# Optimization experiments

Hardware: AMD Instinct MI355X
Metric: run time of the kernel (lower is better)

Reference implementation:

```python
import jax, jax.numpy as jnp
import numpy as np

N_QUBITS = 7
N_LAYERS = 4
DIM = 2 ** N_QUBITS  # 128
# PennyLane StronglyEntanglingLayers default ranges: (l % (n_wires-1)) + 1
RANGES = [(l % (N_QUBITS - 1)) + 1 for l in range(N_LAYERS)]  # [1,2,3,4]
BATCH = 262144


def rot_matrix(phi, theta, omega):
    """PennyLane Rot(phi, theta, omega) = RZ(omega) RY(theta) RZ(phi)."""
    c = jnp.cos(theta / 2)
    s = jnp.sin(theta / 2)
    a = jnp.exp(-0.5j * (phi + omega)) * c
    b = -jnp.exp(0.5j * (phi - omega)) * s
    cc = jnp.exp(-0.5j * (phi - omega)) * s
    d = jnp.exp(0.5j * (phi + omega)) * c
    return jnp.stack([jnp.stack([a, b]), jnp.stack([cc, d])])  # (2,2) complex64


def apply_1q(psi, U, wire):
    # psi: (batch, 2,2,2,2,2,2,2); apply 2x2 U on qubit axis 1+wire
    psi = jnp.moveaxis(psi, 1 + wire, -1)
    psi = psi @ U.T
    return jnp.moveaxis(psi, -1, 1 + wire)


def apply_cnot(psi, ctrl, tgt):
    psi = jnp.moveaxis(psi, (1 + ctrl, 1 + tgt), (-2, -1))
    # flip target amplitude pair where control == 1
    psi = jnp.concatenate([psi[..., 0:1, :], psi[..., 1:2, ::-1]], axis=-2)
    return jnp.moveaxis(psi, (-2, -1), (1 + ctrl, 1 + tgt))


def setup_inputs() -> dict:
    key = jax.random.key(0)
    k1, k2 = jax.random.split(key)
    x = jax.random.normal(k1, (BATCH, DIM), dtype=jnp.float32)
    weights = jax.random.normal(k2, (N_LAYERS, N_QUBITS, 3), dtype=jnp.float32)
    return {"x": x, "weights": weights}


def reference(x, weights):
    # AmplitudeEmbedding with normalize=True
    norm = jnp.linalg.norm(x, axis=-1, keepdims=True)
    psi = (x / norm).astype(jnp.complex64)
    psi = psi.reshape((-1,) + (2,) * N_QUBITS)

    # StronglyEntanglingLayers
    for l in range(N_LAYERS):
        for w in range(N_QUBITS):
            U = rot_matrix(weights[l, w, 0], weights[l, w, 1], weights[l, w, 2])
            psi = apply_1q(psi, U, w)
        r = RANGES[l]
        for w in range(N_QUBITS):
            psi = apply_cnot(psi, w, (w + r) % N_QUBITS)

    # expval(Z0 @ Z6): sign = (-1)^(b0 + b6)
    probs = (jnp.abs(psi) ** 2).reshape(-1, 2, DIM // 4, 2)  # (batch, q0, mid, q6)
    z = jnp.array([1.0, -1.0], dtype=jnp.float32)
    return jnp.einsum('a,namb,b->n', z, probs, z)
```

## Files before the change

### kernel.cpp

```cpp
#include <hip/hip_runtime.h>


#define N_QUBITS 7
#define DIM 128
#define N_LAYERS 4
#define BATCH 262144
#define GRID 512
#define ROWS 32
#define ITERS (BATCH / (GRID * ROWS))

typedef short short8 __attribute__((ext_vector_type(8)));
typedef float f32x4 __attribute__((ext_vector_type(4)));
typedef unsigned int u32;
typedef __attribute__((address_space(1))) const u32 g_u32;
typedef __attribute__((address_space(3))) u32 l_u32;

__device__ __forceinline__ unsigned short f2bf(float f) {
  unsigned u = __builtin_bit_cast(unsigned, f);
  u += 0x7fffu + ((u >> 16) & 1u);
  return (unsigned short)(u >> 16);
}

__device__ __forceinline__ unsigned pk2(float x, float y) {
  unsigned ux = __builtin_bit_cast(unsigned, x) + 0x8000u;
  unsigned uy = __builtin_bit_cast(unsigned, y) + 0x8000u;
  return __builtin_amdgcn_perm(uy, ux, 0x07060302u);
}

__device__ __forceinline__ short8 pack_bf16(float4 lo, float4 hi) {
  uint4 d;
  d.x = pk2(lo.x, lo.y);
  d.y = pk2(lo.z, lo.w);
  d.z = pk2(hi.x, hi.y);
  d.w = pk2(hi.z, hi.w);
  return __builtin_bit_cast(short8, d);
}

__global__ void sim_columns(const float* __restrict__ W,
                            float* __restrict__ Ur, float* __restrict__ Ui) {
  __shared__ float sr[DIM], si[DIM];
  const int c = blockIdx.x;
  const int t = threadIdx.x;

  sr[t] = (t == c) ? 1.f : 0.f;        si[t] = 0.f;
  sr[t + 64] = (t + 64 == c) ? 1.f : 0.f;  si[t + 64] = 0.f;
  __syncthreads();

  for (int l = 0; l < N_LAYERS; ++l) {
    for (int w = 0; w < N_QUBITS; ++w) {
      const float phi = W[(l * 7 + w) * 3 + 0];
      const float th  = W[(l * 7 + w) * 3 + 1];
      const float om  = W[(l * 7 + w) * 3 + 2];
      const float ch = __cosf(0.5f * th), sh = __sinf(0.5f * th);
      const float ap = 0.5f * (phi + om), am = 0.5f * (phi - om);
      const float cap = __cosf(ap), sap = __sinf(ap);
      const float cam = __cosf(am), sam = __sinf(am);
      const float ar =  cap * ch, ai = -sap * ch;
      const float br = -cam * sh, bi = -sam * sh;
      const float cr =  cam * sh, ci = -sam * sh;
      const float dr =  cap * ch, di =  sap * ch;

      const int m = 1 << (6 - w);
      const int i0 = ((t & ~(m - 1)) << 1) | (t & (m - 1));
      const int i1 = i0 | m;
      const float x0r = sr[i0], x0i = si[i0];
      const float x1r = sr[i1], x1i = si[i1];
      __syncthreads();
      sr[i0] = ar * x0r - ai * x0i + br * x1r - bi * x1i;
      si[i0] = ar * x0i + ai * x0r + br * x1i + bi * x1r;
      sr[i1] = cr * x0r - ci * x0i + dr * x1r - di * x1i;
      si[i1] = cr * x0i + ci * x0r + dr * x1i + di * x1r;
      __syncthreads();
    }
    const int r = (l % (N_QUBITS - 1)) + 1;
    for (int w = 0; w < N_QUBITS; ++w) {
      const int ctrl = w, tgt = (w + r) % N_QUBITS;
      const int cmask = 1 << (6 - ctrl), tmask = 1 << (6 - tgt);
      const int i0 = ((t & ~(tmask - 1)) << 1) | (t & (tmask - 1));
      const int i1 = i0 | tmask;
      const float a0r = sr[i0], a0i = si[i0];
      const float a1r = sr[i1], a1i = si[i1];
      __syncthreads();
      if (i0 & cmask) {
        sr[i0] = a1r; si[i0] = a1i;
        sr[i1] = a0r; si[i1] = a0i;
      }
      __syncthreads();
    }
  }
  Ur[(size_t)t * DIM + c]        = sr[t];
  Ui[(size_t)t * DIM + c]        = si[t];
  Ur[(size_t)(t + 64) * DIM + c] = sr[t + 64];
  Ui[(size_t)(t + 64) * DIM + c] = si[t + 64];
}

__global__ void build_A(const float* __restrict__ Ur, const float* __restrict__ Ui,
                        unsigned short* __restrict__ Ab) {
  const int i = blockIdx.x;
  const int j = threadIdx.x;
  float s = 0.f;
#pragma unroll 8
  for (int k = 0; k < DIM; ++k) {
    const float zk = (((k >> 6) ^ k) & 1) ? -1.f : 1.f;
    s += zk * (Ur[k * DIM + i] * Ur[k * DIM + j] + Ui[k * DIM + i] * Ui[k * DIM + j]);
  }
  Ab[i * DIM + j] = f2bf(s);
}

__device__ __forceinline__ void stage_tile(const float* __restrict__ X, float* XsBuf,
                                           int tile, int tid) {
#pragma unroll
  for (int j = 0; j < 8; ++j) {
    const int s = tid + 128 * j;
    const int row = s >> 5;
    const int c = (s & 31) ^ (row & 7);
    const float* gp = X + (size_t)tile * (ROWS * DIM) + row * DIM + c * 4;
    __builtin_amdgcn_global_load_lds((g_u32*)gp, (l_u32*)(XsBuf + s * 4), 16, 0, 0);
  }
}

__global__ __launch_bounds__(128, 2) void vqa_main(const float* __restrict__ X,
                                                   const unsigned short* __restrict__ Ab,
                                                   float* __restrict__ out) {
  __shared__ unsigned short As[DIM * DIM];
  __shared__ float Xs[2 * ROWS * DIM];

  const int tid = threadIdx.x;
  const int lane = tid & 63;
  const int wave = tid >> 6;
  const int n16 = lane & 15;
  const int g = lane >> 4;

  stage_tile(X, Xs, blockIdx.x, tid);

#pragma unroll
  for (int i = 0; i < 16; ++i) {
    const int q = tid + 128 * i;
    const int m = q >> 4, c = q & 15;
    const short8 v = *reinterpret_cast<const short8*>(Ab + q * 8);
    *reinterpret_cast<short8*>(As + m * DIM + ((c ^ (m & 15)) << 3)) = v;
  }

  const unsigned short* abase[4];
#pragma unroll
  for (int kt = 0; kt < 4; ++kt)
    abase[kt] = As + n16 * DIM + (((4 * kt + g) ^ n16) << 3);

  const int R = 16 * wave + n16;
  const int rx = R & 7;

#pragma unroll 1
  for (int it = 0; it < ITERS; ++it) {
    const int cur = it & 1;
    const int rb = cur * (ROWS * 32) + R * 32;

    asm volatile("s_waitcnt vmcnt(0)" ::: "memory");
    __syncthreads();

    short8 bfrag[4];
#pragma unroll
    for (int kt = 0; kt < 4; ++kt) {
      const int c0 = 8 * kt + 2 * g;
      const float4 lo = *reinterpret_cast<const float4*>(Xs + (rb + (c0 ^ rx)) * 4);
      const float4 hi = *reinterpret_cast<const float4*>(Xs + (rb + ((c0 + 1) ^ rx)) * 4);
      bfrag[kt] = pack_bf16(lo, hi);
    }

    if (it + 1 < ITERS)
      stage_tile(X, Xs + (cur ^ 1) * (ROWS * DIM), blockIdx.x + (it + 1) * GRID, tid);

    f32x4 acc[8];
#pragma unroll
    for (int t = 0; t < 8; ++t) acc[t] = (f32x4){0.f, 0.f, 0.f, 0.f};
#pragma unroll
    for (int kt = 0; kt < 4; ++kt) {
#pragma unroll
      for (int t = 0; t < 8; ++t) {
        const short8 af = *reinterpret_cast<const short8*>(abase[kt] + t * 16 * DIM);
        acc[t] = __builtin_amdgcn_mfma_f32_16x16x32_bf16(af, bfrag[kt], acc[t], 0, 0, 0);
      }
    }

    float dot = 0.f, nrm = 0.f;
#pragma unroll
    for (int t = 0; t < 8; ++t) {
      const float4 xe = *reinterpret_cast<const float4*>(Xs + (rb + ((4 * t + g) ^ rx)) * 4);
      dot += xe.x * acc[t][0] + xe.y * acc[t][1] + xe.z * acc[t][2] + xe.w * acc[t][3];
      nrm += xe.x * xe.x + xe.y * xe.y + xe.z * xe.z + xe.w * xe.w;
    }
    dot += __shfl_xor(dot, 16, 64);
    dot += __shfl_xor(dot, 32, 64);
    nrm += __shfl_xor(nrm, 16, 64);
    nrm += __shfl_xor(nrm, 32, 64);
    if (lane < 16) out[(blockIdx.x + it * GRID) * ROWS + R] = dot / nrm;
  }
}

extern "C" void kernel_launch(void* const* d_in, const int* in_sizes, int n_in,
                              void* d_out, int out_size, void* d_ws, size_t ws_size,
                              hipStream_t stream) {
  const float* X = (const float*)d_in[0];
  const float* W = (const float*)d_in[1];
  float* out = (float*)d_out;

  float* Ur = (float*)d_ws;
  float* Ui = Ur + DIM * DIM;
  unsigned short* Ab = (unsigned short*)(Ui + DIM * DIM);

  sim_columns<<<DIM, 64, 0, stream>>>(W, Ur, Ui);
  build_A<<<DIM, DIM, 0, stream>>>(Ur, Ui, Ab);
  vqa_main<<<GRID, 128, 0, stream>>>(X, Ab, out);
}
```

Measured before the change: 205.3 us.

## Load X rows directly from global into MFMA fragments, dropping LDS staging

Drops the double-buffered global_load_lds staging of X tiles and the block-wide barriers. Each wave now reads its 16 rows straight from global memory into bf16 B fragments and computes the norm from those same loads. The launch moves to 1024 blocks of 256 threads, four independent waves per block, and adds a barrier after the A matrix is loaded into LDS. Uncoalesced per-lane row reads and a second global read of x in the epilogue rely on the cache and higher occupancy to hide latency, in place of explicit prefetch.

```diff
diff --git a/kernel.cpp b/kernel.cpp
--- a/kernel.cpp
+++ b/kernel.cpp
@@ -5,15 +5,12 @@
 #define DIM 128
 #define N_LAYERS 4
 #define BATCH 262144
-#define GRID 512
-#define ROWS 32
-#define ITERS (BATCH / (GRID * ROWS))
+#define GRID 1024
+#define WAVES_TOT (GRID * 4)
+#define WITERS (BATCH / 16 / WAVES_TOT)
 
 typedef short short8 __attribute__((ext_vector_type(8)));
 typedef float f32x4 __attribute__((ext_vector_type(4)));
-typedef unsigned int u32;
-typedef __attribute__((address_space(1))) const u32 g_u32;
-typedef __attribute__((address_space(3))) u32 l_u32;
 
 __device__ __forceinline__ unsigned short f2bf(float f) {
   unsigned u = __builtin_bit_cast(unsigned, f);
@@ -107,23 +104,10 @@
   Ab[i * DIM + j] = f2bf(s);
 }
 
-__device__ __forceinline__ void stage_tile(const float* __restrict__ X, float* XsBuf,
-                                           int tile, int tid) {
-#pragma unroll
-  for (int j = 0; j < 8; ++j) {
-    const int s = tid + 128 * j;
-    const int row = s >> 5;
-    const int c = (s & 31) ^ (row & 7);
-    const float* gp = X + (size_t)tile * (ROWS * DIM) + row * DIM + c * 4;
-    __builtin_amdgcn_global_load_lds((g_u32*)gp, (l_u32*)(XsBuf + s * 4), 16, 0, 0);
-  }
-}
-
-__global__ __launch_bounds__(128, 2) void vqa_main(const float* __restrict__ X,
+__global__ __launch_bounds__(256, 3) void vqa_main(const float* __restrict__ X,
                                                    const unsigned short* __restrict__ Ab,
                                                    float* __restrict__ out) {
   __shared__ unsigned short As[DIM * DIM];
-  __shared__ float Xs[2 * ROWS * DIM];
 
   const int tid = threadIdx.x;
   const int lane = tid & 63;
@@ -131,43 +115,37 @@
   const int n16 = lane & 15;
   const int g = lane >> 4;
 
-  stage_tile(X, Xs, blockIdx.x, tid);
-
 #pragma unroll
-  for (int i = 0; i < 16; ++i) {
-    const int q = tid + 128 * i;
+  for (int i = 0; i < 8; ++i) {
+    const int q = tid + 256 * i;
     const int m = q >> 4, c = q & 15;
     const short8 v = *reinterpret_cast<const short8*>(Ab + q * 8);
     *reinterpret_cast<short8*>(As + m * DIM + ((c ^ (m & 15)) << 3)) = v;
   }
+  __syncthreads();
 
   const unsigned short* abase[4];
 #pragma unroll
   for (int kt = 0; kt < 4; ++kt)
     abase[kt] = As + n16 * DIM + (((4 * kt + g) ^ n16) << 3);
 
-  const int R = 16 * wave + n16;
-  const int rx = R & 7;
+  const int wid = blockIdx.x * 4 + wave;
 
 #pragma unroll 1
-  for (int it = 0; it < ITERS; ++it) {
-    const int cur = it & 1;
-    const int rb = cur * (ROWS * 32) + R * 32;
-
-    asm volatile("s_waitcnt vmcnt(0)" ::: "memory");
-    __syncthreads();
+  for (int it = 0; it < WITERS; ++it) {
+    const int row = (wid + it * WAVES_TOT) * 16 + n16;
+    const float* xp = X + (size_t)row * DIM;
 
     short8 bfrag[4];
+    float nrm = 0.f;
 #pragma unroll
     for (int kt = 0; kt < 4; ++kt) {
-      const int c0 = 8 * kt + 2 * g;
-      const float4 lo = *reinterpret_cast<const float4*>(Xs + (rb + (c0 ^ rx)) * 4);
-      const float4 hi = *reinterpret_cast<const float4*>(Xs + (rb + ((c0 + 1) ^ rx)) * 4);
+      const float4 lo = *reinterpret_cast<const float4*>(xp + kt * 32 + g * 8);
+      const float4 hi = *reinterpret_cast<const float4*>(xp + kt * 32 + g * 8 + 4);
+      nrm += lo.x * lo.x + lo.y * lo.y + lo.z * lo.z + lo.w * lo.w;
+      nrm += hi.x * hi.x + hi.y * hi.y + hi.z * hi.z + hi.w * hi.w;
       bfrag[kt] = pack_bf16(lo, hi);
     }
-
-    if (it + 1 < ITERS)
-      stage_tile(X, Xs + (cur ^ 1) * (ROWS * DIM), blockIdx.x + (it + 1) * GRID, tid);
 
     f32x4 acc[8];
 #pragma unroll
@@ -181,18 +159,17 @@
       }
     }
 
-    float dot = 0.f, nrm = 0.f;
+    float dot = 0.f;
 #pragma unroll
     for (int t = 0; t < 8; ++t) {
-      const float4 xe = *reinterpret_cast<const float4*>(Xs + (rb + ((4 * t + g) ^ rx)) * 4);
+      const float4 xe = *reinterpret_cast<const float4*>(xp + t * 16 + g * 4);
       dot += xe.x * acc[t][0] + xe.y * acc[t][1] + xe.z * acc[t][2] + xe.w * acc[t][3];
-      nrm += xe.x * xe.x + xe.y * xe.y + xe.z * xe.z + xe.w * xe.w;
     }
     dot += __shfl_xor(dot, 16, 64);
     dot += __shfl_xor(dot, 32, 64);
     nrm += __shfl_xor(nrm, 16, 64);
     nrm += __shfl_xor(nrm, 32, 64);
-    if (lane < 16) out[(blockIdx.x + it * GRID) * ROWS + R] = dot / nrm;
+    if (lane < 16) out[row] = dot / nrm;
   }
 }
 
@@ -209,5 +186,5 @@
 
   sim_columns<<<DIM, 64, 0, stream>>>(W, Ur, Ui);
   build_A<<<DIM, DIM, 0, stream>>>(Ur, Ui, Ab);
-  vqa_main<<<GRID, 128, 0, stream>>>(X, Ab, out);
+  vqa_main<<<GRID, 256, 0, stream>>>(X, Ab, out);
 }
```

Result: slower. 288.0 us (+40.3%).
